# Kernel tuning notes

Measured on AMD Instinct MI355X. Metric: run time of the kernel, lower is better.

Reference implementation:

```python
import jax, jax.numpy as jnp
import numpy as np

NEG = -1000000000.0

def setup_inputs() -> dict:
    key = jax.random.key(0)
    k1, k2 = jax.random.split(key)
    b, t, d, k = 32, 4096, 512, 8
    h = jax.random.normal(k1, (b, t, d), dtype=jnp.float32)
    mask = jnp.ones((b, t), dtype=bool)
    queries = jax.random.normal(k2, (k, d), dtype=jnp.float32)
    return {"h": h, "mask": mask, "queries": queries}

def reference(h, mask, queries):
    # attn scores: (b, k, t), no scaling
    attn = jnp.einsum('kd,btd->bkt', queries, h)
    attn = jnp.where(mask[:, None, :], attn, NEG)
    attn = jax.nn.softmax(attn, axis=-1)
    slots = jnp.einsum('bkt,btd->bkd', attn, h)
    return slots
```

## Files before the change

### kernel.cpp

```cpp
#include <hip/hip_runtime.h>
#include <hip/hip_bf16.h>


#define NEGV -1000000000.0f

constexpr int B = 32;
constexpr int T = 4096;
constexpr int D = 512;
constexpr int K = 8;
constexpr float SHIFT = 80.0f;

typedef unsigned int u32x2 __attribute__((ext_vector_type(2)));

__device__ __forceinline__ float rdlane(float v, int l) {
  return __uint_as_float(__builtin_amdgcn_readlane(__float_as_uint(v), l));
}

__device__ __forceinline__ void pl32swap(float& a, float& b) {
  u32x2 r = __builtin_amdgcn_permlane32_swap(
      __float_as_uint(a), __float_as_uint(b), false, false);
  a = __uint_as_float(r[0]);
  b = __uint_as_float(r[1]);
}

__device__ __forceinline__ void pl16swap(float& a, float& b) {
  u32x2 r = __builtin_amdgcn_permlane16_swap(
      __float_as_uint(a), __float_as_uint(b), false, false);
  a = __uint_as_float(r[0]);
  b = __uint_as_float(r[1]);
}

template <int CTRL>
__device__ __forceinline__ float dppmov(float x) {
  return __uint_as_float(__builtin_amdgcn_update_dpp(
      __float_as_uint(x), __float_as_uint(x), CTRL, 0xF, 0xF, true));
}

__device__ __forceinline__ void load_grp(const float* __restrict__ hb,
                                         const int* __restrict__ mb, int t,
                                         float (&hv)[2][8], int2& mk) {
  int tt = (t <= T - 2) ? t : (T - 2);
#pragma unroll
  for (int rr = 0; rr < 2; ++rr) {
    const float4 a = *(const float4*)(hb + (size_t)(tt + rr) * D);
    const float4 c = *(const float4*)(hb + (size_t)(tt + rr) * D + 4);
    hv[rr][0] = a.x; hv[rr][1] = a.y; hv[rr][2] = a.z; hv[rr][3] = a.w;
    hv[rr][4] = c.x; hv[rr][5] = c.y; hv[rr][6] = c.z; hv[rr][7] = c.w;
  }
  mk = *(const int2*)(mb + tt);
}

__device__ __forceinline__ void compute_grp(
    const float (&hv)[2][8], const int2 mk, const float (&qv)[4][8],
    float (&acc)[4][8], float& llane, bool c5, bool c3) {
  float v[8];
#pragma unroll
  for (int rr = 0; rr < 2; ++rr)
#pragma unroll
    for (int ss = 0; ss < 4; ++ss) {
      float a = 0.f;
#pragma unroll
      for (int j = 0; j < 8; ++j) a = fmaf(qv[ss][j], hv[rr][j], a);
      v[rr * 4 + ss] = a;
    }

  pl32swap(v[0], v[4]); float u0 = v[0] + v[4];
  pl32swap(v[1], v[5]); float u1 = v[1] + v[5];
  pl32swap(v[2], v[6]); float u2 = v[2] + v[6];
  pl32swap(v[3], v[7]); float u3 = v[3] + v[7];

  pl16swap(u0, u2); float x02 = u0 + u2;
  pl16swap(u1, u3); float x13 = u1 + u3;

  x02 += dppmov<0x128>(x02);
  x13 += dppmov<0x128>(x13);
  float y = c3 ? x13 : x02;

  y += dppmov<0xB1>(y);
  y += dppmov<0x4E>(y);
  y += dppmov<0x141>(y);

  const int mrow = c5 ? mk.y : mk.x;
  const float s = mrow ? y : NEGV;

  const float el = __expf(s - SHIFT);
  llane += el;

  const float e0 = rdlane(el, 0),  e1 = rdlane(el, 8);
  const float e2 = rdlane(el, 16), e3 = rdlane(el, 24);
  const float e4 = rdlane(el, 32), e5 = rdlane(el, 40);
  const float e6 = rdlane(el, 48), e7 = rdlane(el, 56);
#pragma unroll
  for (int j = 0; j < 8; ++j) {
    acc[0][j] = fmaf(e0, hv[0][j], acc[0][j]);
    acc[1][j] = fmaf(e1, hv[0][j], acc[1][j]);
    acc[2][j] = fmaf(e2, hv[0][j], acc[2][j]);
    acc[3][j] = fmaf(e3, hv[0][j], acc[3][j]);
    acc[0][j] = fmaf(e4, hv[1][j], acc[0][j]);
    acc[1][j] = fmaf(e5, hv[1][j], acc[1][j]);
    acc[2][j] = fmaf(e6, hv[1][j], acc[2][j]);
    acc[3][j] = fmaf(e7, hv[1][j], acc[3][j]);
  }
}

__global__ __launch_bounds__(256, 4) void pool_pass1(
    const float* __restrict__ h, const int* __restrict__ mask,
    const float* __restrict__ q, float* __restrict__ wsacc,
    float* __restrict__ wsl, int nchunks, int rows) {
  const int chunk = blockIdx.x;
  const int b = blockIdx.y;
  const int tid = threadIdx.x;
  const int wave = tid >> 6;
  const int lane = tid & 63;
  const int sg = wave & 1;
  const int half = wave >> 1;
  const int dbase = lane * 8;
  const int rowsw = rows >> 1;
  const int t0 = chunk * rows + half * rowsw;
  const bool c5 = (lane & 32) != 0;
  const bool c3 = (lane & 8) != 0;

  float qv[4][8];
#pragma unroll
  for (int ss = 0; ss < 4; ++ss) {
    const float* qp = q + (size_t)(sg * 4 + ss) * D + dbase;
    const float4 a = *(const float4*)(qp);
    const float4 c = *(const float4*)(qp + 4);
    qv[ss][0]=a.x; qv[ss][1]=a.y; qv[ss][2]=a.z; qv[ss][3]=a.w;
    qv[ss][4]=c.x; qv[ss][5]=c.y; qv[ss][6]=c.z; qv[ss][7]=c.w;
  }

  float acc[4][8] = {};
  float llane = 0.f;

  const float* hb = h + (size_t)b * T * D + dbase;
  const int* mb = mask + (size_t)b * T;

  float hvA[2][8], hvB[2][8];
  int2 mkA, mkB;

  load_grp(hb, mb, t0, hvA, mkA);
  for (int g = 0; g < rowsw; g += 4) {
    load_grp(hb, mb, t0 + g + 2, hvB, mkB);
    compute_grp(hvA, mkA, qv, acc, llane, c5, c3);
    load_grp(hb, mb, t0 + g + 4, hvA, mkA);
    compute_grp(hvB, mkB, qv, acc, llane, c5, c3);
  }

  float lr = llane;
  lr += __shfl_xor(lr, 32, 64);
  lr += __shfl_xor(lr, 4, 64);
  lr += __shfl_xor(lr, 2, 64);
  lr += __shfl_xor(lr, 1, 64);
  float l[4];
#pragma unroll
  for (int ss = 0; ss < 4; ++ss) l[ss] = 0.125f * rdlane(lr, 8 * ss);

  __shared__ float so[2][4][D];
  __shared__ float sl[2][4];
  if (half == 1) {
#pragma unroll
    for (int ss = 0; ss < 4; ++ss) {
      float4 o;
      o.x=acc[ss][0]; o.y=acc[ss][1]; o.z=acc[ss][2]; o.w=acc[ss][3];
      *(float4*)(&so[sg][ss][dbase]) = o;
      o.x=acc[ss][4]; o.y=acc[ss][5]; o.z=acc[ss][6]; o.w=acc[ss][7];
      *(float4*)(&so[sg][ss][dbase + 4]) = o;
    }
    if (lane < 4) sl[sg][lane] = l[lane];
  }
  __syncthreads();
  if (half == 0) {
    size_t pbase = ((size_t)(b * nchunks + chunk) * K + sg * 4);
#pragma unroll
    for (int ss = 0; ss < 4; ++ss) {
      float* ap = wsacc + (pbase + ss) * D + dbase;
      float4 o;
      o.x = acc[ss][0] + so[sg][ss][dbase + 0];
      o.y = acc[ss][1] + so[sg][ss][dbase + 1];
      o.z = acc[ss][2] + so[sg][ss][dbase + 2];
      o.w = acc[ss][3] + so[sg][ss][dbase + 3];
      *(float4*)(ap) = o;
      o.x = acc[ss][4] + so[sg][ss][dbase + 4];
      o.y = acc[ss][5] + so[sg][ss][dbase + 5];
      o.z = acc[ss][6] + so[sg][ss][dbase + 6];
      o.w = acc[ss][7] + so[sg][ss][dbase + 7];
      *(float4*)(ap + 4) = o;
    }
    if (lane < 4) wsl[pbase + lane] = l[lane] + sl[sg][lane];
  }
}

__global__ __launch_bounds__(256) void pool_pass2(
    const float* __restrict__ wsacc, const float* __restrict__ wsl,
    float* __restrict__ out, int nchunks) {
  const int bk = blockIdx.x;
  const int tid = threadIdx.x;
  const int wave = tid >> 6;
  const int lane = tid & 63;
  const int b = bk >> 3;
  const int k = bk & 7;

  __shared__ float so[4][D];
  __shared__ float sl[4];

  float o[8] = {0,0,0,0,0,0,0,0};
  float lsum = 0.f;
  for (int c = wave; c < nchunks; c += 4) {
    size_t idx = (size_t)(b * nchunks + c) * K + k;
    const float* ap = wsacc + idx * D + lane * 8;
    float4 a0 = *(const float4*)(ap);
    float4 a1 = *(const float4*)(ap + 4);
    o[0] += a0.x; o[1] += a0.y; o[2] += a0.z; o[3] += a0.w;
    o[4] += a1.x; o[5] += a1.y; o[6] += a1.z; o[7] += a1.w;
    lsum += wsl[idx];
  }
#pragma unroll
  for (int j = 0; j < 8; ++j) so[wave][lane * 8 + j] = o[j];
  if (lane == 0) sl[wave] = lsum;
  __syncthreads();

  const float L = sl[0] + sl[1] + sl[2] + sl[3];
  const float inv = 1.0f / L;
  const int d2 = tid * 2;
  float r0 = so[0][d2] + so[1][d2] + so[2][d2] + so[3][d2];
  float r1 = so[0][d2 + 1] + so[1][d2 + 1] + so[2][d2 + 1] + so[3][d2 + 1];
  float2 v;
  v.x = r0 * inv;
  v.y = r1 * inv;
  *(float2*)(out + (size_t)bk * D + d2) = v;
}

extern "C" void kernel_launch(void* const* d_in, const int* in_sizes, int n_in,
                              void* d_out, int out_size, void* d_ws, size_t ws_size,
                              hipStream_t stream) {
  const float* h = (const float*)d_in[0];
  const int* mask = (const int*)d_in[1];
  const float* q = (const float*)d_in[2];
  float* out = (float*)d_out;

  int nc = 64;
  while (nc > 1 &&
         (size_t)B * nc * K * (D + 1) * sizeof(float) > ws_size)
    nc >>= 1;

  float* wsacc = (float*)d_ws;
  float* wsl = wsacc + (size_t)B * nc * K * D;

  dim3 g1(nc, B);
  pool_pass1<<<g1, 256, 0, stream>>>(h, mask, q, wsacc, wsl, nc, T / nc);
  pool_pass2<<<B * K, 256, 0, stream>>>(wsacc, wsl, out, nc);
}
```

Before: 69.46 us.

## Process one row per step with 3-deep prefetch and simpler cross-lane reduction

Each step now handles one h row instead of a pair. The cross-lane reduction shrinks to two permlane swaps plus four DPP adds and needs no lane-select. The loads are restructured as a rotating 4-buffer pipeline with three rows in flight, and the l-sum readout drops the extra shuffle reduction. The goal is fewer reduction instructions per score and better latency hiding of global loads. The cost is more serial readlane/exp chains per row and more live registers.

```diff
diff --git a/kernel.cpp b/kernel.cpp
--- a/kernel.cpp
+++ b/kernel.cpp
@@ -36,70 +36,50 @@
       __float_as_uint(x), __float_as_uint(x), CTRL, 0xF, 0xF, true));
 }
 
-__device__ __forceinline__ void load_grp(const float* __restrict__ hb,
+__device__ __forceinline__ void load_row(const float* __restrict__ hb,
                                          const int* __restrict__ mb, int t,
-                                         float (&hv)[2][8], int2& mk) {
-  int tt = (t <= T - 2) ? t : (T - 2);
-#pragma unroll
-  for (int rr = 0; rr < 2; ++rr) {
-    const float4 a = *(const float4*)(hb + (size_t)(tt + rr) * D);
-    const float4 c = *(const float4*)(hb + (size_t)(tt + rr) * D + 4);
-    hv[rr][0] = a.x; hv[rr][1] = a.y; hv[rr][2] = a.z; hv[rr][3] = a.w;
-    hv[rr][4] = c.x; hv[rr][5] = c.y; hv[rr][6] = c.z; hv[rr][7] = c.w;
-  }
-  mk = *(const int2*)(mb + tt);
-}
-
-__device__ __forceinline__ void compute_grp(
-    const float (&hv)[2][8], const int2 mk, const float (&qv)[4][8],
-    float (&acc)[4][8], float& llane, bool c5, bool c3) {
-  float v[8];
-#pragma unroll
-  for (int rr = 0; rr < 2; ++rr)
-#pragma unroll
-    for (int ss = 0; ss < 4; ++ss) {
-      float a = 0.f;
-#pragma unroll
-      for (int j = 0; j < 8; ++j) a = fmaf(qv[ss][j], hv[rr][j], a);
-      v[rr * 4 + ss] = a;
-    }
-
-  pl32swap(v[0], v[4]); float u0 = v[0] + v[4];
-  pl32swap(v[1], v[5]); float u1 = v[1] + v[5];
-  pl32swap(v[2], v[6]); float u2 = v[2] + v[6];
-  pl32swap(v[3], v[7]); float u3 = v[3] + v[7];
-
-  pl16swap(u0, u2); float x02 = u0 + u2;
-  pl16swap(u1, u3); float x13 = u1 + u3;
-
-  x02 += dppmov<0x128>(x02);
-  x13 += dppmov<0x128>(x13);
-  float y = c3 ? x13 : x02;
-
+                                         int tend, float (&hv)[8], int& mk) {
+  const int tt = (t < tend) ? t : (tend - 1);
+  const float4 a = *(const float4*)(hb + (size_t)tt * D);
+  const float4 c = *(const float4*)(hb + (size_t)tt * D + 4);
+  hv[0] = a.x; hv[1] = a.y; hv[2] = a.z; hv[3] = a.w;
+  hv[4] = c.x; hv[5] = c.y; hv[6] = c.z; hv[7] = c.w;
+  mk = mb[tt];
+}
+
+__device__ __forceinline__ void compute_row(const float (&hv)[8], int mk,
+                                            const float (&qv)[4][8],
+                                            float (&acc)[4][8],
+                                            float& llane) {
+  float v0 = 0.f, v1 = 0.f, v2 = 0.f, v3 = 0.f;
+#pragma unroll
+  for (int j = 0; j < 8; ++j) {
+    v0 = fmaf(qv[0][j], hv[j], v0);
+    v1 = fmaf(qv[1][j], hv[j], v1);
+    v2 = fmaf(qv[2][j], hv[j], v2);
+    v3 = fmaf(qv[3][j], hv[j], v3);
+  }
+
+  pl32swap(v0, v2); float u02 = v0 + v2;
+  pl32swap(v1, v3); float u13 = v1 + v3;
+  pl16swap(u02, u13); float y = u02 + u13;
+  y += dppmov<0x128>(y);
   y += dppmov<0xB1>(y);
   y += dppmov<0x4E>(y);
   y += dppmov<0x141>(y);
 
-  const int mrow = c5 ? mk.y : mk.x;
-  const float s = mrow ? y : NEGV;
-
+  const float s = mk ? y : NEGV;
   const float el = __expf(s - SHIFT);
   llane += el;
 
-  const float e0 = rdlane(el, 0),  e1 = rdlane(el, 8);
-  const float e2 = rdlane(el, 16), e3 = rdlane(el, 24);
-  const float e4 = rdlane(el, 32), e5 = rdlane(el, 40);
-  const float e6 = rdlane(el, 48), e7 = rdlane(el, 56);
+  const float e0 = rdlane(el, 0),  e1 = rdlane(el, 16);
+  const float e2 = rdlane(el, 32), e3 = rdlane(el, 48);
 #pragma unroll
   for (int j = 0; j < 8; ++j) {
-    acc[0][j] = fmaf(e0, hv[0][j], acc[0][j]);
-    acc[1][j] = fmaf(e1, hv[0][j], acc[1][j]);
-    acc[2][j] = fmaf(e2, hv[0][j], acc[2][j]);
-    acc[3][j] = fmaf(e3, hv[0][j], acc[3][j]);
-    acc[0][j] = fmaf(e4, hv[1][j], acc[0][j]);
-    acc[1][j] = fmaf(e5, hv[1][j], acc[1][j]);
-    acc[2][j] = fmaf(e6, hv[1][j], acc[2][j]);
-    acc[3][j] = fmaf(e7, hv[1][j], acc[3][j]);
+    acc[0][j] = fmaf(e0, hv[j], acc[0][j]);
+    acc[1][j] = fmaf(e1, hv[j], acc[1][j]);
+    acc[2][j] = fmaf(e2, hv[j], acc[2][j]);
+    acc[3][j] = fmaf(e3, hv[j], acc[3][j]);
   }
 }
 
@@ -117,8 +97,7 @@
   const int dbase = lane * 8;
   const int rowsw = rows >> 1;
   const int t0 = chunk * rows + half * rowsw;
-  const bool c5 = (lane & 32) != 0;
-  const bool c3 = (lane & 8) != 0;
+  const int tend = t0 + rowsw;
 
   float qv[4][8];
 #pragma unroll
@@ -136,25 +115,26 @@
   const float* hb = h + (size_t)b * T * D + dbase;
   const int* mb = mask + (size_t)b * T;
 
-  float hvA[2][8], hvB[2][8];
-  int2 mkA, mkB;
-
-  load_grp(hb, mb, t0, hvA, mkA);
+  float hv0[8], hv1[8], hv2[8], hv3[8];
+  int mk0, mk1, mk2, mk3;
+
+  load_row(hb, mb, t0 + 0, tend, hv0, mk0);
+  load_row(hb, mb, t0 + 1, tend, hv1, mk1);
+  load_row(hb, mb, t0 + 2, tend, hv2, mk2);
   for (int g = 0; g < rowsw; g += 4) {
-    load_grp(hb, mb, t0 + g + 2, hvB, mkB);
-    compute_grp(hvA, mkA, qv, acc, llane, c5, c3);
-    load_grp(hb, mb, t0 + g + 4, hvA, mkA);
-    compute_grp(hvB, mkB, qv, acc, llane, c5, c3);
-  }
-
-  float lr = llane;
-  lr += __shfl_xor(lr, 32, 64);
-  lr += __shfl_xor(lr, 4, 64);
-  lr += __shfl_xor(lr, 2, 64);
-  lr += __shfl_xor(lr, 1, 64);
+    load_row(hb, mb, t0 + g + 3, tend, hv3, mk3);
+    compute_row(hv0, mk0, qv, acc, llane);
+    load_row(hb, mb, t0 + g + 4, tend, hv0, mk0);
+    compute_row(hv1, mk1, qv, acc, llane);
+    load_row(hb, mb, t0 + g + 5, tend, hv1, mk1);
+    compute_row(hv2, mk2, qv, acc, llane);
+    load_row(hb, mb, t0 + g + 6, tend, hv2, mk2);
+    compute_row(hv3, mk3, qv, acc, llane);
+  }
+
   float l[4];
 #pragma unroll
-  for (int ss = 0; ss < 4; ++ss) l[ss] = 0.125f * rdlane(lr, 8 * ss);
+  for (int ss = 0; ss < 4; ++ss) l[ss] = rdlane(llane, 16 * ss);
 
   __shared__ float so[2][4][D];
   __shared__ float sl[2][4];
```

Measured after the change: 66.51 us. 4.2% less time.
